# Kernel optimization log

Measured on AMD Instinct MI355X. Metric: run time of the kernel, lower is better.

The kernel has to match this reference:

```python
import jax, jax.numpy as jnp
import numpy as np

TEMP = 0.1
COEFF = 0.5
WARMUP = 0
S = 32 * 32  # hardcoded in the torch module


def _l2n(x, axis):
    # matches F.normalize(p=2, eps=1e-12)
    n = jnp.linalg.norm(x, axis=axis, keepdims=True)
    return x / jnp.maximum(n, 1e-12)


def _ce_first_class(pos, neg):
    # cross-entropy with label 0 on logits = [pos | neg] / T
    logits = jnp.concatenate([pos, neg], axis=1) / TEMP
    return jnp.mean(jax.nn.logsumexp(logits, axis=1) - logits[:, 0])


def _dense_losses(q_of, q_x, k_of, k_x, k_avg_dense):
    # q_of,k_of: (B,d,S) normalized; q_x,k_x: (B,C,S) normalized; k_avg_dense: (B,C) UN-normalized (torch bug preserved)
    B, C, _ = q_x.shape
    sim = jnp.einsum('bds,bdt->bst', q_of, k_of)          # (B,S,S)
    ind = jnp.argmax(sim, axis=2)                          # (B,S)
    idxg = jnp.take_along_axis(k_x, jnp.broadcast_to(ind[:, None, :], k_x.shape), axis=2)
    idxg = jax.lax.stop_gradient(idxg)                     # computed under torch.no_grad
    l_pos = jnp.sum(q_x * idxg, axis=1).reshape(-1, 1)     # (B*S,1)
    qf = jnp.transpose(q_x, (0, 2, 1)).reshape(-1, C)      # (B*S,C)
    l_neg_full = qf @ k_avg_dense.T                        # (B*S,B)
    # static mask: row n excludes column n // S
    base = np.stack([np.delete(np.arange(B), i) for i in range(B)])  # (B,B-1)
    neg_cols = jnp.asarray(np.repeat(base, S, axis=0))     # (B*S,B-1)
    l_neg = jnp.take_along_axis(l_neg_full, neg_cols, axis=1)
    return l_pos, l_neg


def _forward(original_features_q, avgpooled_global_q, x_q, avgpooled_dense_q,
             original_features_k, avgpooled_global_k, x_k, avgpooled_dense_k, epoch):
    of = jnp.concatenate([original_features_q, original_features_k], axis=0)
    ag = jnp.concatenate([avgpooled_global_q, avgpooled_global_k], axis=0)
    x = jnp.concatenate([x_q, x_k], axis=0)
    ad = jnp.concatenate([avgpooled_dense_q, avgpooled_dense_k], axis=0)

    # global InfoNCE
    agn = _l2n(ag, 1)
    sim = agn @ agn.T                                      # (2B,2B)
    n2 = sim.shape[0]
    B = n2 // 2
    rows = np.arange(n2)
    pos_cols = (rows + B) % n2
    pos = sim[jnp.asarray(rows), jnp.asarray(pos_cols)][:, None]
    neg_cols = np.stack([np.setdiff1d(rows, [i, pos_cols[i]]) for i in range(n2)])  # (2B,2B-2)
    neg = jnp.take_along_axis(sim, jnp.asarray(neg_cols), axis=1)
    global_loss = _ce_first_class(pos, neg)

    # dense InfoNCE
    b, d, h, w = of.shape
    of = _l2n(of.reshape(b, d, h * w), 1)
    xn = _l2n(x, 1)
    q_of, k_of = of[:b // 2], of[b // 2:]
    q_x, k_x = xn[:b // 2], xn[b // 2:]
    q_ad, k_ad = ad[:b // 2], ad[b // 2:]  # NOTE: un-normalized, matching the torch code
    p1, n1 = _dense_losses(q_of, q_x, k_of, k_x, k_ad)
    p2, n2_ = _dense_losses(k_of, k_x, q_of, q_x, q_ad)
    dense_loss = _ce_first_class(jnp.concatenate([p1, p2], axis=0),
                                 jnp.concatenate([n1, n2_], axis=0))

    if epoch > WARMUP:
        return COEFF * global_loss + (1.0 - COEFF) * dense_loss
    return global_loss


def setup_inputs() -> dict:
    key = jax.random.key(0)
    ks = jax.random.split(key, 8)
    B, d, C, h, w = 64, 256, 128, 32, 32
    return {
        'original_features_q': jax.random.normal(ks[0], (B, d, h, w), jnp.float32),
        'avgpooled_global_q': jax.random.normal(ks[1], (B, C), jnp.float32),
        'x_q': jax.random.normal(ks[2], (B, C, h * w), jnp.float32),
        'avgpooled_dense_q': jax.random.normal(ks[3], (B, C), jnp.float32),
        'original_features_k': jax.random.normal(ks[4], (B, d, h, w), jnp.float32),
        'avgpooled_global_k': jax.random.normal(ks[5], (B, C), jnp.float32),
        'x_k': jax.random.normal(ks[6], (B, C, h * w), jnp.float32),
        'avgpooled_dense_k': jax.random.normal(ks[7], (B, C), jnp.float32),
        'epoch': 5,
    }


def reference(original_features_q, avgpooled_global_q, x_q, avgpooled_dense_q,
              original_features_k, avgpooled_global_k, x_k, avgpooled_dense_k, epoch):
    return _forward(original_features_q, avgpooled_global_q, x_q, avgpooled_dense_q,
                    original_features_k, avgpooled_global_k, x_k, avgpooled_dense_k, epoch)
```

## Files before the change

kernel.cpp:

```cpp
#include <hip/hip_runtime.h>
#include <math.h>

#define TEMP_INV 10.0f

typedef unsigned long long u64;
typedef __attribute__((ext_vector_type(8))) __bf16 bf16x8;
typedef __attribute__((ext_vector_type(4))) float f32x4;

__device__ inline unsigned fkey(float v) {
  unsigned u = __float_as_uint(v);
  return (u & 0x80000000u) ? ~u : (u | 0x80000000u);
}

__device__ __forceinline__ void async_copy16(const void* gp, void* lp) {
  __builtin_amdgcn_global_load_lds(
      (__attribute__((address_space(1))) void*)(unsigned long long)gp,
      (__attribute__((address_space(3))) void*)(unsigned long long)lp,
      16, 0, 0);
}

__global__ __launch_bounds__(256) void kcvt(const float* __restrict__ ofq,
                                            const float* __restrict__ ofk,
                                            __bf16* __restrict__ ofT,
                                            float* __restrict__ of_invn) {
  int s0 = blockIdx.x * 32, b = blockIdx.y;
  const float* src = (b < 64) ? (ofq + (size_t)b * 262144) : (ofk + (size_t)(b - 64) * 262144);
  __shared__ __bf16 T[32][36];
  __shared__ float R[8][32];
  int t = threadIdx.x;
  int dd = t >> 5, ss = t & 31;
  int wr = t >> 3, wd = t & 7;
  float ssq = 0.f;
  __bf16* out = ofT + (size_t)b * 262144 + (size_t)s0 * 256;
  for (int d0 = 0; d0 < 256; d0 += 32) {
    float v[4];
#pragma unroll
    for (int it = 0; it < 4; ++it) {
      int d = d0 + dd + 8 * it;
      v[it] = src[(size_t)d * 1024 + s0 + ss];
      ssq += v[it] * v[it];
    }
    __syncthreads();
#pragma unroll
    for (int it = 0; it < 4; ++it) T[ss][dd + 8 * it] = (__bf16)v[it];
    __syncthreads();
    *(uint2*)(out + (size_t)wr * 256 + d0 + wd * 4) = *(const uint2*)(&T[wr][wd * 4]);
  }
  R[dd][ss] = ssq;
  __syncthreads();
  if (t < 32) {
    float a = 0.f;
#pragma unroll
    for (int r = 0; r < 8; ++r) a += R[r][t];
    of_invn[b * 1024 + s0 + t] = 1.0f / fmaxf(sqrtf(a), 1e-12f);
  }
}

__global__ void kprep(const float* __restrict__ xq, const float* __restrict__ xk,
                      float* __restrict__ x_invn,
                      const float* __restrict__ adq, const float* __restrict__ adk,
                      float* __restrict__ adt) {
  if (blockIdx.x < 512) {
    int idx = blockIdx.x * 256 + threadIdx.x;
    int b = idx >> 10, s = idx & 1023;
    const float* src = (b < 64) ? (xq + (size_t)b * 131072) : (xk + (size_t)(b - 64) * 131072);
    float acc = 0.f;
#pragma unroll 8
    for (int c = 0; c < 128; ++c) { float v = src[c * 1024 + s]; acc += v * v; }
    x_invn[idx] = 1.0f / fmaxf(sqrtf(acc), 1e-12f);
  } else {
    int i = (blockIdx.x - 512) * 256 + threadIdx.x;
    int dir = i >> 13, r = i & 8191;
    int j = r >> 7, c = r & 127;
    const float* ad = dir == 0 ? adk : adq;
    adt[dir * 8192 + c * 64 + j] = ad[j * 128 + c];
  }
}

__global__ __launch_bounds__(512, 2) void ksim(
    const __bf16* __restrict__ ofT, const float* __restrict__ of_invn,
    u64* __restrict__ best_row, u64* __restrict__ best_col) {
  unsigned h = blockIdx.x + (blockIdx.y << 2) + (blockIdx.z << 4);
  int xcd = h & 7;
  unsigned slot = h >> 3;
  int b = xcd + 8 * (int)(slot >> 4);
  int tile = slot & 15;
  int s0 = (tile & 3) * 256, t0 = (tile >> 2) * 256;

  const __bf16* Ag = ofT + (size_t)b * 262144;
  const __bf16* Bg = ofT + (size_t)(b + 64) * 262144;
  __shared__ __bf16 As[2][16384];
  __shared__ __bf16 Bs[2][16384];

  int t = threadIdx.x;
  int lane = t & 63, w = t >> 6;
  int lc = lane & 15, q = lane >> 4;
  int wm = w >> 2, wn = w & 3;

  f32x4 acc[8][4];
#pragma unroll
  for (int i = 0; i < 8; ++i)
#pragma unroll
    for (int j = 0; j < 4; ++j) acc[i][j] = (f32x4)(0.f);

  int aoff[8], boff[4];
#pragma unroll
  for (int i = 0; i < 8; ++i) {
    int mr = wm * 128 + i * 16 + lc;
    aoff[i] = mr * 64 + ((q ^ (mr & 7)) << 3);
  }
#pragma unroll
  for (int j = 0; j < 4; ++j) {
    int nc = wn * 64 + j * 16 + lc;
    boff[j] = nc * 64 + ((q ^ (nc & 7)) << 3);
  }

  int ms = t >> 3, gphys = t & 7;
  int lg = gphys ^ (ms & 7);
  size_t aSrc = (size_t)(s0 + ms) * 256 + lg * 8;
  size_t bSrc = (size_t)(t0 + ms) * 256 + lg * 8;

  auto STAGE = [&](int bufn, int k0) {
    char* aL = (char*)&As[bufn][0] + t * 16;
    char* bL = (char*)&Bs[bufn][0] + t * 16;
#pragma unroll
    for (int c = 0; c < 4; ++c) {
      async_copy16(Ag + aSrc + (size_t)c * 16384 + k0, aL + c * 8192);
      async_copy16(Bg + bSrc + (size_t)c * 16384 + k0, bL + c * 8192);
    }
  };

  STAGE(0, 0);
  __syncthreads();

  for (int it = 0; it < 4; ++it) {
    int buf = it & 1;
    if (it < 3) STAGE(buf ^ 1, (it + 1) * 64);
#pragma unroll
    for (int kk = 0; kk < 2; ++kk) {
      int kx = kk << 5;
      bf16x8 af[8], bfr[4];
#pragma unroll
      for (int i = 0; i < 8; ++i) af[i] = *(const bf16x8*)(&As[buf][0] + (aoff[i] ^ kx));
#pragma unroll
      for (int j = 0; j < 4; ++j) bfr[j] = *(const bf16x8*)(&Bs[buf][0] + (boff[j] ^ kx));
      __builtin_amdgcn_s_setprio(1);
#pragma unroll
      for (int i = 0; i < 8; ++i)
#pragma unroll
        for (int j = 0; j < 4; ++j)
          acc[i][j] = __builtin_amdgcn_mfma_f32_16x16x32_bf16(af[i], bfr[j], acc[i][j], 0, 0, 0);
      __builtin_amdgcn_s_setprio(0);
    }
    __syncthreads();
  }

  float sk[4];
#pragma unroll
  for (int j = 0; j < 4; ++j) sk[j] = of_invn[65536 + b * 1024 + t0 + wn * 64 + j * 16 + lc];
  float sq[32];
#pragma unroll
  for (int i = 0; i < 8; ++i)
#pragma unroll
    for (int e = 0; e < 4; ++e)
      sq[i * 4 + e] = of_invn[b * 1024 + s0 + wm * 128 + i * 16 + q * 4 + e];

  u64* browb = best_row + (size_t)b * 1024 + s0;
  u64* bcolb = best_col + (size_t)b * 1024 + t0;

#pragma unroll
  for (int i = 0; i < 8; ++i) {
#pragma unroll
    for (int e = 0; e < 4; ++e) {
      float v[4];
#pragma unroll
      for (int j = 0; j < 4; ++j) v[j] = acc[i][j][e] * sk[j];
      float vb = fmaxf(fmaxf(v[0], v[1]), fmaxf(v[2], v[3]));
#pragma unroll
      for (int mask = 1; mask <= 8; mask <<= 1) vb = fmaxf(vb, __shfl_xor(vb, mask));
      unsigned ib = 0xFFFFFFFFu;
#pragma unroll
      for (int j = 0; j < 4; ++j) {
        unsigned cand = (v[j] == vb) ? (unsigned)(t0 + wn * 64 + j * 16 + lc) : 0xFFFFFFFFu;
        ib = min(ib, cand);
      }
#pragma unroll
      for (int mask = 1; mask <= 8; mask <<= 1) ib = min(ib, __shfl_xor(ib, mask));
      if (lc == 0)
        atomicMax(browb + wm * 128 + i * 16 + q * 4 + e,
                  ((u64)fkey(vb) << 32) | (u64)(0xFFFFFFFFu - ib));
    }
  }

#pragma unroll
  for (int j = 0; j < 4; ++j) {
    float cb = -INFINITY;
#pragma unroll
    for (int i = 0; i < 8; ++i)
#pragma unroll
      for (int e = 0; e < 4; ++e) cb = fmaxf(cb, acc[i][j][e] * sq[i * 4 + e]);
    cb = fmaxf(cb, __shfl_xor(cb, 16));
    cb = fmaxf(cb, __shfl_xor(cb, 32));
    unsigned ib = 0xFFFFFFFFu;
#pragma unroll
    for (int i = 0; i < 8; ++i)
#pragma unroll
      for (int e = 0; e < 4; ++e) {
        float m2 = acc[i][j][e] * sq[i * 4 + e];
        unsigned cand = (m2 == cb) ? (unsigned)(s0 + wm * 128 + i * 16 + q * 4 + e) : 0xFFFFFFFFu;
        ib = min(ib, cand);
      }
    ib = min(ib, __shfl_xor(ib, 16));
    ib = min(ib, __shfl_xor(ib, 32));
    if (lane < 16)
      atomicMax(bcolb + wn * 64 + j * 16 + lane,
                ((u64)fkey(cb) << 32) | (u64)(0xFFFFFFFFu - ib));
  }
}

__global__ __launch_bounds__(1024) void kpos(
    const float* __restrict__ xq, const float* __restrict__ xk,
    const float* __restrict__ x_invn,
    const u64* __restrict__ best_row, const u64* __restrict__ best_col,
    float* __restrict__ posl) {
  int b = blockIdx.x, dir = blockIdx.y;
  const float* xsrc = dir == 0 ? xq : xk;
  const float* xdst = dir == 0 ? xk : xq;
  const float* inv_src = x_invn + (dir ? 65536 : 0);
  const float* inv_dst = x_invn + (dir ? 0 : 65536);
  const u64* best = dir == 0 ? best_row : best_col;

  __shared__ float xrow[8][1024];
  __shared__ float sdinv[1024];
  int t = threadIdx.x;
  sdinv[t] = inv_dst[b * 1024 + t];
  u64 p = best[(size_t)b * 1024 + t];
  int sidx = (int)(0xFFFFFFFFu - (unsigned)(p & 0xFFFFFFFFull));
  const float* xsb = xsrc + (size_t)b * 131072;
  const float* xdb = xdst + (size_t)b * 131072;
  float acc = 0.f;
  for (int c0 = 0; c0 < 128; c0 += 8) {
    __syncthreads();
#pragma unroll
    for (int qq = 0; qq < 2; ++qq)
      ((float4*)xrow)[t + 1024 * qq] = ((const float4*)(xdb + (size_t)c0 * 1024))[t + 1024 * qq];
    __syncthreads();
#pragma unroll
    for (int cc = 0; cc < 8; ++cc)
      acc += xsb[(size_t)(c0 + cc) * 1024 + t] * xrow[cc][sidx];
  }
  posl[dir * 65536 + b * 1024 + t] = acc * inv_src[b * 1024 + t] * sdinv[sidx] * TEMP_INV;
}

__global__ __launch_bounds__(256) void kneg(
    const float* __restrict__ xq, const float* __restrict__ xk,
    const float* __restrict__ x_invn,
    const float* __restrict__ adt, const float* __restrict__ posl,
    float* __restrict__ dsum) {
  int st = blockIdx.x, b = blockIdx.y, dir = blockIdx.z;
  const float* xsrc = dir == 0 ? xq : xk;
  const float* inv_src = x_invn + (dir ? 65536 : 0);
  const float* Bt = adt + dir * 8192;

  __shared__ float As2[64][64];
  __shared__ float Bs2[128][64];
  __shared__ float red[16];

  int tid = threadIdx.x;
  int tx = tid & 15, ty = tid >> 4;
  int s0 = st * 64;

#pragma unroll
  for (int qq = 0; qq < 8; ++qq)
    reinterpret_cast<float4*>(Bs2)[tid + 256 * qq] =
        reinterpret_cast<const float4*>(Bt)[tid + 256 * qq];

  float acc[4][4];
#pragma unroll
  for (int i = 0; i < 4; ++i)
#pragma unroll
    for (int j = 0; j < 4; ++j) acc[i][j] = 0.f;

  int lm = tid & 63, lk = tid >> 6;
  float sinv = inv_src[b * 1024 + s0 + lm];
  const float* xb = xsrc + (size_t)b * 131072;

  for (int k0 = 0; k0 < 128; k0 += 64) {
#pragma unroll
    for (int r = 0; r < 16; ++r) {
      int kk = lk + 4 * r;
      As2[kk][lm] = xb[(k0 + kk) * 1024 + s0 + lm] * sinv;
    }
    __syncthreads();
#pragma unroll
    for (int kk = 0; kk < 64; ++kk) {
      float4 av = *reinterpret_cast<const float4*>(&As2[kk][ty * 4]);
      float4 bv = *reinterpret_cast<const float4*>(&Bs2[k0 + kk][tx * 4]);
      float a[4] = {av.x, av.y, av.z, av.w};
      float bb[4] = {bv.x, bv.y, bv.z, bv.w};
#pragma unroll
      for (int i = 0; i < 4; ++i)
#pragma unroll
        for (int j = 0; j < 4; ++j) acc[i][j] += a[i] * bb[j];
    }
    __syncthreads();
  }

  float lsum = 0.f;
#pragma unroll
  for (int i = 0; i < 4; ++i) {
    int s = s0 + ty * 4 + i;
    float pos = posl[dir * 65536 + b * 1024 + s];
    float lg[4];
    float mloc = -INFINITY;
#pragma unroll
    for (int j = 0; j < 4; ++j) {
      int jg = tx * 4 + j;
      lg[j] = (jg == b) ? -INFINITY : acc[i][j] * TEMP_INV;
      mloc = fmaxf(mloc, lg[j]);
    }
#pragma unroll
    for (int mask = 1; mask <= 8; mask <<= 1) mloc = fmaxf(mloc, __shfl_xor(mloc, mask));
    float m = fmaxf(mloc, pos);
    float e = 0.f;
#pragma unroll
    for (int j = 0; j < 4; ++j) e += __expf(lg[j] - m);
#pragma unroll
    for (int mask = 1; mask <= 8; mask <<= 1) e += __shfl_xor(e, mask);
    if (tx == 0) lsum += m + __logf(e + __expf(pos - m)) - pos;
  }
  if (tx == 0) red[ty] = lsum;
  __syncthreads();
  if (tid == 0) {
    float v = 0.f;
#pragma unroll
    for (int r = 0; r < 16; ++r) v += red[r];
    atomicAdd(dsum, v);
  }
}

__global__ void kglobal(const float* __restrict__ agq, const float* __restrict__ agk,
                        float* __restrict__ gsum) {
  __shared__ float logits[128];
  __shared__ float rinv[128];
  int i = blockIdx.x, j = threadIdx.x;
  const float* rowi = (i < 64) ? (agq + i * 128) : (agk + (i - 64) * 128);
  const float* rowj = (j < 64) ? (agq + j * 128) : (agk + (j - 64) * 128);
  float dot = 0.f, nj = 0.f;
#pragma unroll 8
  for (int c = 0; c < 128; ++c) { float a = rowi[c], bb = rowj[c]; dot += a * bb; nj += bb * bb; }
  rinv[j] = 1.0f / fmaxf(sqrtf(nj), 1e-12f);
  __syncthreads();
  logits[j] = dot * rinv[i] * rinv[j] * TEMP_INV;
  __syncthreads();
  if (j == 0) {
    int pos = (i + 64) & 127;
    float m = -INFINITY;
    for (int t = 0; t < 128; ++t) if (t != i) m = fmaxf(m, logits[t]);
    float e = 0.f;
    for (int t = 0; t < 128; ++t) if (t != i) e += __expf(logits[t] - m);
    atomicAdd(gsum, m + __logf(e) - logits[pos]);
  }
}

__global__ void kfinal(const float* __restrict__ gsum, const float* __restrict__ dsum,
                       const int* __restrict__ epoch, float* __restrict__ out) {
  if (threadIdx.x == 0) {
    float g = gsum[0] / 128.0f;
    float dn = dsum[0] / 131072.0f;
    out[0] = (epoch[0] > 0) ? (0.5f * g + 0.5f * dn) : g;
  }
}

extern "C" void kernel_launch(void* const* d_in, const int* in_sizes, int n_in,
                              void* d_out, int out_size, void* d_ws, size_t ws_size,
                              hipStream_t stream) {
  const float* ofq = (const float*)d_in[0];
  const float* agq = (const float*)d_in[1];
  const float* xq  = (const float*)d_in[2];
  const float* adq = (const float*)d_in[3];
  const float* ofk = (const float*)d_in[4];
  const float* agk = (const float*)d_in[5];
  const float* xk  = (const float*)d_in[6];
  const float* adk = (const float*)d_in[7];
  const int* epoch = (const int*)d_in[8];
  float* out = (float*)d_out;

  char* wsb = (char*)d_ws;
  __bf16* ofT = (__bf16*)wsb;
  u64* best_row = (u64*)(wsb + 67108864);
  u64* best_col = best_row + 65536;
  float* gsum = (float*)(best_col + 65536);
  float* dsum = gsum + 1;
  float* posl = dsum + 1;
  float* x_invn  = posl + 131072;
  float* of_invn = x_invn + 131072;
  float* adt = of_invn + 131072;

  hipMemsetAsync(best_row, 0, 65536ull * 8 * 2 + 8, stream);

  dim3 gc(32, 128);
  kcvt<<<gc, 256, 0, stream>>>(ofq, ofk, ofT, of_invn);
  kprep<<<576, 256, 0, stream>>>(xq, xk, x_invn, adq, adk, adt);
  kglobal<<<128, 128, 0, stream>>>(agq, agk, gsum);

  dim3 gs(4, 4, 64);
  ksim<<<gs, 512, 0, stream>>>(ofT, of_invn, best_row, best_col);

  dim3 gp(64, 2);
  kpos<<<gp, 1024, 0, stream>>>(xq, xk, x_invn, best_row, best_col, posl);

  dim3 gn(16, 64, 2);
  kneg<<<gn, 256, 0, stream>>>(xq, xk, x_invn, adt, posl, dsum);

  kfinal<<<1, 1, 0, stream>>>(gsum, dsum, epoch, out);
}
```

Baseline: 399.1 us.

## Fuse preprocessing kernels, split kpos into halves, drop LDS tiling in kneg

The three preprocessing kernels (bf16 transpose/convert, norm and transpose prep, global InfoNCE) are merged into one launch with block-range dispatch, which removes two launch gaps. kpos now uses 512-thread blocks over a doubled grid, so each block handles half the spatial positions and more blocks run at once. The cost is that the xrow tile is staged into LDS twice per (b, dir). kneg drops its shared-memory staging and reads A and B directly from global memory with float4 loads, removing barriers but relying on cache for reuse.

Result: slower. 416.6 us (+4.4%).

```diff
diff --git a/kernel.cpp b/kernel.cpp
--- a/kernel.cpp
+++ b/kernel.cpp
@@ -19,61 +19,87 @@
       16, 0, 0);
 }
 
-__global__ __launch_bounds__(256) void kcvt(const float* __restrict__ ofq,
-                                            const float* __restrict__ ofk,
-                                            __bf16* __restrict__ ofT,
-                                            float* __restrict__ of_invn) {
-  int s0 = blockIdx.x * 32, b = blockIdx.y;
-  const float* src = (b < 64) ? (ofq + (size_t)b * 262144) : (ofk + (size_t)(b - 64) * 262144);
-  __shared__ __bf16 T[32][36];
-  __shared__ float R[8][32];
+__global__ __launch_bounds__(256) void kpre(
+    const float* __restrict__ ofq, const float* __restrict__ ofk,
+    __bf16* __restrict__ ofT, float* __restrict__ of_invn,
+    const float* __restrict__ xq, const float* __restrict__ xk,
+    float* __restrict__ x_invn,
+    const float* __restrict__ adq, const float* __restrict__ adk,
+    float* __restrict__ adt,
+    const float* __restrict__ agq, const float* __restrict__ agk,
+    float* __restrict__ gsum) {
+  unsigned bx = blockIdx.x;
   int t = threadIdx.x;
-  int dd = t >> 5, ss = t & 31;
-  int wr = t >> 3, wd = t & 7;
-  float ssq = 0.f;
-  __bf16* out = ofT + (size_t)b * 262144 + (size_t)s0 * 256;
-  for (int d0 = 0; d0 < 256; d0 += 32) {
-    float v[4];
-#pragma unroll
-    for (int it = 0; it < 4; ++it) {
-      int d = d0 + dd + 8 * it;
-      v[it] = src[(size_t)d * 1024 + s0 + ss];
-      ssq += v[it] * v[it];
-    }
-    __syncthreads();
-#pragma unroll
-    for (int it = 0; it < 4; ++it) T[ss][dd + 8 * it] = (__bf16)v[it];
-    __syncthreads();
-    *(uint2*)(out + (size_t)wr * 256 + d0 + wd * 4) = *(const uint2*)(&T[wr][wd * 4]);
-  }
-  R[dd][ss] = ssq;
-  __syncthreads();
-  if (t < 32) {
-    float a = 0.f;
-#pragma unroll
-    for (int r = 0; r < 8; ++r) a += R[r][t];
-    of_invn[b * 1024 + s0 + t] = 1.0f / fmaxf(sqrtf(a), 1e-12f);
-  }
-}
-
-__global__ void kprep(const float* __restrict__ xq, const float* __restrict__ xk,
-                      float* __restrict__ x_invn,
-                      const float* __restrict__ adq, const float* __restrict__ adk,
-                      float* __restrict__ adt) {
-  if (blockIdx.x < 512) {
-    int idx = blockIdx.x * 256 + threadIdx.x;
-    int b = idx >> 10, s = idx & 1023;
-    const float* src = (b < 64) ? (xq + (size_t)b * 131072) : (xk + (size_t)(b - 64) * 131072);
-    float acc = 0.f;
+  if (bx < 4096) {
+    int s0 = (bx & 31) * 32, b = bx >> 5;
+    const float* src = (b < 64) ? (ofq + (size_t)b * 262144) : (ofk + (size_t)(b - 64) * 262144);
+    __shared__ __bf16 T[32][36];
+    __shared__ float R[8][32];
+    int dd = t >> 5, ss = t & 31;
+    int wr = t >> 3, wd = t & 7;
+    float ssq = 0.f;
+    __bf16* out = ofT + (size_t)b * 262144 + (size_t)s0 * 256;
+    for (int d0 = 0; d0 < 256; d0 += 32) {
+      float v[4];
+#pragma unroll
+      for (int it = 0; it < 4; ++it) {
+        int d = d0 + dd + 8 * it;
+        v[it] = src[(size_t)d * 1024 + s0 + ss];
+        ssq += v[it] * v[it];
+      }
+      __syncthreads();
+#pragma unroll
+      for (int it = 0; it < 4; ++it) T[ss][dd + 8 * it] = (__bf16)v[it];
+      __syncthreads();
+      *(uint2*)(out + (size_t)wr * 256 + d0 + wd * 4) = *(const uint2*)(&T[wr][wd * 4]);
+    }
+    R[dd][ss] = ssq;
+    __syncthreads();
+    if (t < 32) {
+      float a = 0.f;
+#pragma unroll
+      for (int r = 0; r < 8; ++r) a += R[r][t];
+      of_invn[b * 1024 + s0 + t] = 1.0f / fmaxf(sqrtf(a), 1e-12f);
+    }
+  } else if (bx < 4672) {
+    unsigned px = bx - 4096;
+    if (px < 512) {
+      int idx = px * 256 + t;
+      int b = idx >> 10, s = idx & 1023;
+      const float* src = (b < 64) ? (xq + (size_t)b * 131072) : (xk + (size_t)(b - 64) * 131072);
+      float acc = 0.f;
 #pragma unroll 8
-    for (int c = 0; c < 128; ++c) { float v = src[c * 1024 + s]; acc += v * v; }
-    x_invn[idx] = 1.0f / fmaxf(sqrtf(acc), 1e-12f);
+      for (int c = 0; c < 128; ++c) { float v = src[c * 1024 + s]; acc += v * v; }
+      x_invn[idx] = 1.0f / fmaxf(sqrtf(acc), 1e-12f);
+    } else {
+      int i = (px - 512) * 256 + t;
+      int dir = i >> 13, r = i & 8191;
+      int j = r >> 7, c = r & 127;
+      const float* ad = dir == 0 ? adk : adq;
+      adt[dir * 8192 + c * 64 + j] = ad[j * 128 + c];
+    }
   } else {
-    int i = (blockIdx.x - 512) * 256 + threadIdx.x;
-    int dir = i >> 13, r = i & 8191;
-    int j = r >> 7, c = r & 127;
-    const float* ad = dir == 0 ? adk : adq;
-    adt[dir * 8192 + c * 64 + j] = ad[j * 128 + c];
+    __shared__ float logits[2][128];
+    __shared__ float rinv[128];
+    int ii = t >> 7, j = t & 127;
+    int i = (int)(bx - 4672) * 2 + ii;
+    const float* rowi = (i < 64) ? (agq + i * 128) : (agk + (i - 64) * 128);
+    const float* rowj = (j < 64) ? (agq + j * 128) : (agk + (j - 64) * 128);
+    float dot = 0.f, nj = 0.f;
+#pragma unroll 8
+    for (int c = 0; c < 128; ++c) { float a = rowi[c], bb = rowj[c]; dot += a * bb; nj += bb * bb; }
+    if (ii == 0) rinv[j] = 1.0f / fmaxf(sqrtf(nj), 1e-12f);
+    __syncthreads();
+    logits[ii][j] = dot * rinv[i] * rinv[j] * TEMP_INV;
+    __syncthreads();
+    if (j == 0) {
+      int pos = (i + 64) & 127;
+      float m = -INFINITY;
+      for (int tt = 0; tt < 128; ++tt) if (tt != i) m = fmaxf(m, logits[ii][tt]);
+      float e = 0.f;
+      for (int tt = 0; tt < 128; ++tt) if (tt != i) e += __expf(logits[ii][tt] - m);
+      atomicAdd(gsum, m + __logf(e) - logits[ii][pos]);
+    }
   }
 }
 
@@ -218,12 +244,12 @@
   }
 }
 
-__global__ __launch_bounds__(1024) void kpos(
+__global__ __launch_bounds__(512) void kpos(
     const float* __restrict__ xq, const float* __restrict__ xk,
     const float* __restrict__ x_invn,
     const u64* __restrict__ best_row, const u64* __restrict__ best_col,
     float* __restrict__ posl) {
-  int b = blockIdx.x, dir = blockIdx.y;
+  int b = blockIdx.x, dir = blockIdx.y, half = blockIdx.z;
   const float* xsrc = dir == 0 ? xq : xk;
   const float* xdst = dir == 0 ? xk : xq;
   const float* inv_src = x_invn + (dir ? 65536 : 0);
@@ -233,8 +259,10 @@
   __shared__ float xrow[8][1024];
   __shared__ float sdinv[1024];
   int t = threadIdx.x;
+  int s = half * 512 + t;
   sdinv[t] = inv_dst[b * 1024 + t];
-  u64 p = best[(size_t)b * 1024 + t];
+  sdinv[t + 512] = inv_dst[b * 1024 + t + 512];
+  u64 p = best[(size_t)b * 1024 + s];
   int sidx = (int)(0xFFFFFFFFu - (unsigned)(p & 0xFFFFFFFFull));
   const float* xsb = xsrc + (size_t)b * 131072;
   const float* xdb = xdst + (size_t)b * 131072;
@@ -242,14 +270,14 @@
   for (int c0 = 0; c0 < 128; c0 += 8) {
     __syncthreads();
 #pragma unroll
-    for (int qq = 0; qq < 2; ++qq)
-      ((float4*)xrow)[t + 1024 * qq] = ((const float4*)(xdb + (size_t)c0 * 1024))[t + 1024 * qq];
+    for (int qq = 0; qq < 4; ++qq)
+      ((float4*)xrow)[t + 512 * qq] = ((const float4*)(xdb + (size_t)c0 * 1024))[t + 512 * qq];
     __syncthreads();
 #pragma unroll
     for (int cc = 0; cc < 8; ++cc)
-      acc += xsb[(size_t)(c0 + cc) * 1024 + t] * xrow[cc][sidx];
-  }
-  posl[dir * 65536 + b * 1024 + t] = acc * inv_src[b * 1024 + t] * sdinv[sidx] * TEMP_INV;
+      acc += xsb[(size_t)(c0 + cc) * 1024 + s] * xrow[cc][sidx];
+  }
+  posl[dir * 65536 + b * 1024 + s] = acc * inv_src[b * 1024 + s] * sdinv[sidx] * TEMP_INV;
 }
 
 __global__ __launch_bounds__(256) void kneg(
@@ -262,18 +290,14 @@
   const float* inv_src = x_invn + (dir ? 65536 : 0);
   const float* Bt = adt + dir * 8192;
 
-  __shared__ float As2[64][64];
-  __shared__ float Bs2[128][64];
   __shared__ float red[16];
 
   int tid = threadIdx.x;
   int tx = tid & 15, ty = tid >> 4;
   int s0 = st * 64;
-
-#pragma unroll
-  for (int qq = 0; qq < 8; ++qq)
-    reinterpret_cast<float4*>(Bs2)[tid + 256 * qq] =
-        reinterpret_cast<const float4*>(Bt)[tid + 256 * qq];
+  const float* xb = xsrc + (size_t)b * 131072;
+
+  float4 sinv4 = *reinterpret_cast<const float4*>(inv_src + b * 1024 + s0 + ty * 4);
 
   float acc[4][4];
 #pragma unroll
@@ -281,29 +305,19 @@
 #pragma unroll
     for (int j = 0; j < 4; ++j) acc[i][j] = 0.f;
 
-  int lm = tid & 63, lk = tid >> 6;
-  float sinv = inv_src[b * 1024 + s0 + lm];
-  const float* xb = xsrc + (size_t)b * 131072;
-
-  for (int k0 = 0; k0 < 128; k0 += 64) {
-#pragma unroll
-    for (int r = 0; r < 16; ++r) {
-      int kk = lk + 4 * r;
-      As2[kk][lm] = xb[(k0 + kk) * 1024 + s0 + lm] * sinv;
-    }
-    __syncthreads();
-#pragma unroll
-    for (int kk = 0; kk < 64; ++kk) {
-      float4 av = *reinterpret_cast<const float4*>(&As2[kk][ty * 4]);
-      float4 bv = *reinterpret_cast<const float4*>(&Bs2[k0 + kk][tx * 4]);
-      float a[4] = {av.x, av.y, av.z, av.w};
-      float bb[4] = {bv.x, bv.y, bv.z, bv.w};
-#pragma unroll
-      for (int i = 0; i < 4; ++i)
-#pragma unroll
-        for (int j = 0; j < 4; ++j) acc[i][j] += a[i] * bb[j];
-    }
-    __syncthreads();
+  const float* arow = xb + s0 + ty * 4;
+  const float* brow = Bt + tx * 4;
+
+#pragma unroll 4
+  for (int kk = 0; kk < 128; ++kk) {
+    float4 av = *reinterpret_cast<const float4*>(arow + (size_t)kk * 1024);
+    float4 bv = *reinterpret_cast<const float4*>(brow + (size_t)kk * 64);
+    float a[4] = {av.x * sinv4.x, av.y * sinv4.y, av.z * sinv4.z, av.w * sinv4.w};
+    float bb[4] = {bv.x, bv.y, bv.z, bv.w};
+#pragma unroll
+    for (int i = 0; i < 4; ++i)
+#pragma unroll
+      for (int j = 0; j < 4; ++j) acc[i][j] += a[i] * bb[j];
   }
 
   float lsum = 0.f;
@@ -336,30 +350,6 @@
 #pragma unroll
     for (int r = 0; r < 16; ++r) v += red[r];
     atomicAdd(dsum, v);
-  }
-}
-
-__global__ void kglobal(const float* __restrict__ agq, const float* __restrict__ agk,
-                        float* __restrict__ gsum) {
-  __shared__ float logits[128];
-  __shared__ float rinv[128];
-  int i = blockIdx.x, j = threadIdx.x;
-  const float* rowi = (i < 64) ? (agq + i * 128) : (agk + (i - 64) * 128);
-  const float* rowj = (j < 64) ? (agq + j * 128) : (agk + (j - 64) * 128);
-  float dot = 0.f, nj = 0.f;
-#pragma unroll 8
-  for (int c = 0; c < 128; ++c) { float a = rowi[c], bb = rowj[c]; dot += a * bb; nj += bb * bb; }
-  rinv[j] = 1.0f / fmaxf(sqrtf(nj), 1e-12f);
-  __syncthreads();
-  logits[j] = dot * rinv[i] * rinv[j] * TEMP_INV;
-  __syncthreads();
-  if (j == 0) {
-    int pos = (i + 64) & 127;
-    float m = -INFINITY;
-    for (int t = 0; t < 128; ++t) if (t != i) m = fmaxf(m, logits[t]);
-    float e = 0.f;
-    for (int t = 0; t < 128; ++t) if (t != i) e += __expf(logits[t] - m);
-    atomicAdd(gsum, m + __logf(e) - logits[pos]);
   }
 }
 
@@ -399,16 +389,14 @@
 
   hipMemsetAsync(best_row, 0, 65536ull * 8 * 2 + 8, stream);
 
-  dim3 gc(32, 128);
-  kcvt<<<gc, 256, 0, stream>>>(ofq, ofk, ofT, of_invn);
-  kprep<<<576, 256, 0, stream>>>(xq, xk, x_invn, adq, adk, adt);
-  kglobal<<<128, 128, 0, stream>>>(agq, agk, gsum);
+  kpre<<<4736, 256, 0, stream>>>(ofq, ofk, ofT, of_invn, xq, xk, x_invn,
+                                 adq, adk, adt, agq, agk, gsum);
 
   dim3 gs(4, 4, 64);
   ksim<<<gs, 512, 0, stream>>>(ofT, of_invn, best_row, best_col);
 
-  dim3 gp(64, 2);
-  kpos<<<gp, 1024, 0, stream>>>(xq, xk, x_invn, best_row, best_col, posl);
+  dim3 gp(64, 2, 2);
+  kpos<<<gp, 512, 0, stream>>>(xq, xk, x_invn, best_row, best_col, posl);
 
   dim3 gn(16, 64, 2);
   kneg<<<gn, 256, 0, stream>>>(xq, xk, x_invn, adt, posl, dsum);
```
